# Optimization experiments

Measured on AMD Instinct MI355X. Metric: run time of the kernel, lower is better.

## Reference

```python
import jax, jax.numpy as jnp
import numpy as np

B, T, D = 4, 2048, 2048
HS, NH, NG = 128, 16, 4  # head_size, n_head, n_query_groups
R = NH // NG             # queries per group


def setup_inputs() -> dict:
    key = jax.random.key(0)
    ks = jax.random.split(key, 8)
    s = 0.02
    return {
        "x": jax.random.normal(ks[0], (B, T, D), dtype=jnp.float32),
        "WQ": jax.random.normal(ks[1], (HS * NH, D), dtype=jnp.float32) * s,
        "bQ": jax.random.normal(ks[2], (HS * NH,), dtype=jnp.float32) * s,
        "WK": jax.random.normal(ks[3], (HS * NG, D), dtype=jnp.float32) * s,
        "bK": jax.random.normal(ks[4], (HS * NG,), dtype=jnp.float32) * s,
        "WV": jax.random.normal(ks[5], (HS * NG, D), dtype=jnp.float32) * s,
        "bV": jax.random.normal(ks[6], (HS * NG,), dtype=jnp.float32) * s,
        "proj": jax.random.normal(ks[7], (HS * NH, D), dtype=jnp.float32) * s,
    }


def reference(x, WQ, bQ, WK, bK, WV, bV, proj):
    b, t, _ = x.shape
    # projections (torch Linear: x @ W.T + b)
    Q = x @ WQ.T + bQ                                   # (B,T,NH*HS)
    K = (x @ WK.T + bK).reshape(b, t, NG, HS)           # (B,T,NG,HS)
    V = (x @ WV.T + bV).reshape(b, t, NG, HS)
    # torch .repeat tiles the group axis: [g0..g3, g0..g3, ...]
    K = jnp.tile(K, (1, 1, R, 1)).reshape(b, t, NH * HS)
    V = jnp.tile(V, (1, 1, R, 1)).reshape(b, t, NH * HS)
    # single big-dim attention over the concatenated head dim (as in source)
    scores = jnp.einsum('btd,bsd->bts', Q, K)           # (B,T,T)
    causal = jnp.triu(jnp.ones((t, t), dtype=bool), 1)
    scores = jnp.where(causal[None], -jnp.inf, scores)
    # quirk: divide by sqrt(head_size) AFTER softmax
    attn = jax.nn.softmax(scores, axis=-1) / jnp.sqrt(jnp.float32(HS))
    Z = jnp.einsum('bts,bsd->btd', attn, V)             # (B,T,NH*HS)
    return Z @ proj                                     # (B,T,D)
```

## Files before the change

kernel.cpp:

```cpp
#include <hip/hip_runtime.h>
#include <math.h>

typedef _Float16 h16;
typedef _Float16 f16x8 __attribute__((ext_vector_type(8)));
typedef _Float16 f16x4 __attribute__((ext_vector_type(4)));
typedef float f32x4 __attribute__((ext_vector_type(4)));

enum { EPI_F32 = 0, EPI_SPLIT2 = 1, EPI_VT = 2, EPI_H16 = 3 };

struct GP {
  const h16* Ah; const h16* Al;
  const h16* Bh; const h16* Bl;
  const float* bias;
  float* outF;
  h16* oQh; h16* oQl; h16* oKh; h16* oKl;
  h16* outH;
  int K, lda, ldb, ldc;
  size_t sA, sB, sO;
};

__device__ __forceinline__ f32x4 mfma16(f16x8 a, f16x8 b, f32x4 c) {
  return __builtin_amdgcn_mfma_f32_16x16x32_f16(a, b, c, 0, 0, 0);
}

__device__ __forceinline__ void glds16(const h16* g, h16* l) {
  __builtin_amdgcn_global_load_lds((const __attribute__((address_space(1))) void*)g,
                                   (__attribute__((address_space(3))) void*)l,
                                   16, 0, 0);
}

template<int BM, int BN, int BSPL, int TERMS, int EPI, bool CSKIP, bool KLIM>
__global__ __launch_bounds__(256, 2) void gemm_bt(GP p)
{
  constexpr int BK = 64;
  constexpr bool ASPL = (TERMS >= 2);
  constexpr int WM = BM / 2, WN = BN / 2;
  constexpr int FM = WM / 16, FN = WN / 16;

  const int gx = gridDim.x, gy = gridDim.y;
  int lin = blockIdx.x + gx * blockIdx.y;
  const int nwg = gx * gy;
  if ((nwg & 7) == 0) lin = (lin & 7) * (nwg >> 3) + (lin >> 3);
  const int m0 = (lin / gx) * BM;
  const int n0 = (lin % gx) * BN;
  if (CSKIP && n0 >= m0 + BM) return;
  const int z = blockIdx.z;
  const h16* Ah = p.Ah + (size_t)z * p.sA;
  const h16* Al = ASPL ? p.Al + (size_t)z * p.sA : (const h16*)nullptr;
  const h16* Bh = p.Bh + (size_t)z * p.sB;
  const h16* Bl = BSPL ? p.Bl + (size_t)z * p.sB : (const h16*)nullptr;

  __shared__ h16 sAh[BM * BK];
  __shared__ h16 sAl[ASPL ? BM * BK : 8];
  __shared__ h16 sBh[BN * BK];
  __shared__ h16 sBl[BSPL ? BN * BK : 8];

  const int tid = threadIdx.x;
  const int lane = tid & 63;
  const int w = tid >> 6;
  const int wm = (w >> 1) * WM;
  const int wn = (w & 1) * WN;
  const int fr = lane & 15;
  const int fq = lane >> 4;
  const int lrow = lane >> 3;
  const int lcol = (((lane & 7) ^ lrow) * 8);

  f32x4 acc[FM][FN];
#pragma unroll
  for (int i = 0; i < FM; i++)
#pragma unroll
    for (int j = 0; j < FN; j++) acc[i][j] = f32x4{0.f, 0.f, 0.f, 0.f};

  const int kend = KLIM ? ((m0 + BM < p.K) ? (m0 + BM) : p.K) : p.K;

  for (int k0 = 0; k0 < kend; k0 += BK) {
    __syncthreads();
#pragma unroll
    for (int i = w; i < BM / 8; i += 4)
      glds16(Ah + (size_t)(m0 + i * 8 + lrow) * p.lda + (k0 + lcol), &sAh[i * 512]);
    if constexpr (ASPL) {
#pragma unroll
      for (int i = w; i < BM / 8; i += 4)
        glds16(Al + (size_t)(m0 + i * 8 + lrow) * p.lda + (k0 + lcol), &sAl[i * 512]);
    }
#pragma unroll
    for (int i = w; i < BN / 8; i += 4)
      glds16(Bh + (size_t)(n0 + i * 8 + lrow) * p.ldb + (k0 + lcol), &sBh[i * 512]);
    if constexpr (BSPL) {
#pragma unroll
      for (int i = w; i < BN / 8; i += 4)
        glds16(Bl + (size_t)(n0 + i * 8 + lrow) * p.ldb + (k0 + lcol), &sBl[i * 512]);
    }
    __syncthreads();

#pragma unroll
    for (int ks = 0; ks < 2; ks++) {
      const int swo = (((ks * 4 + fq) ^ (fr & 7)) * 8);
      f16x8 fa[FM], fb[FN];
      f16x8 fal[ASPL ? FM : 1], fbl[BSPL ? FN : 1];
#pragma unroll
      for (int m = 0; m < FM; m++) {
        fa[m] = *(const f16x8*)&sAh[(wm + m * 16 + fr) * BK + swo];
        if constexpr (ASPL)
          fal[m] = *(const f16x8*)&sAl[(wm + m * 16 + fr) * BK + swo];
      }
#pragma unroll
      for (int n = 0; n < FN; n++) {
        fb[n] = *(const f16x8*)&sBh[(wn + n * 16 + fr) * BK + swo];
        if constexpr (BSPL)
          fbl[n] = *(const f16x8*)&sBl[(wn + n * 16 + fr) * BK + swo];
      }
#pragma unroll
      for (int m = 0; m < FM; m++)
#pragma unroll
        for (int n = 0; n < FN; n++) {
          acc[m][n] = mfma16(fa[m], fb[n], acc[m][n]);
          if constexpr (TERMS >= 2) acc[m][n] = mfma16(fal[m], fb[n], acc[m][n]);
          if constexpr (TERMS >= 3) acc[m][n] = mfma16(fa[m], fbl[n], acc[m][n]);
        }
    }
  }

#pragma unroll
  for (int m = 0; m < FM; m++) {
    const int grb = m0 + wm + m * 16 + fq * 4;
#pragma unroll
    for (int n = 0; n < FN; n++) {
      const int gc = n0 + wn + n * 16 + fr;
      if constexpr (EPI == EPI_F32) {
        float* o = p.outF + (size_t)z * p.sO;
#pragma unroll
        for (int r = 0; r < 4; r++)
          o[(size_t)(grb + r) * p.ldc + gc] = acc[m][n][r];
      } else if constexpr (EPI == EPI_SPLIT2) {
        const float bv = p.bias[gc];
#pragma unroll
        for (int r = 0; r < 4; r++) {
          const float v = acc[m][n][r] + bv;
          const h16 h = (h16)v;
          const h16 l = (h16)(v - (float)h);
          const size_t idx = (size_t)(grb + r) * 512;
          if (gc < 512) { p.oQh[idx + gc] = h; p.oQl[idx + gc] = l; }
          else          { p.oKh[idx + gc - 512] = h; p.oKl[idx + gc - 512] = l; }
        }
      } else if constexpr (EPI == EPI_VT) {
        const float bv = p.bias[gc];
        f16x4 pk;
#pragma unroll
        for (int r = 0; r < 4; r++) pk[r] = (h16)(acc[m][n][r] + bv);
        const int bb = grb >> 11;
        const int t  = grb & 2047;
        *(f16x4*)(p.outH + ((size_t)bb * 512 + gc) * 2048 + t) = pk;
      } else {
        h16* o = p.outH + (size_t)z * p.sO;
#pragma unroll
        for (int r = 0; r < 4; r++)
          o[(size_t)(grb + r) * p.ldc + gc] = (h16)acc[m][n][r];
      }
    }
  }
}

__global__ __launch_bounds__(256) void split_x(const float* __restrict__ x,
                                               h16* __restrict__ xh, h16* __restrict__ xl)
{
  const size_t i = ((size_t)blockIdx.x * 256 + threadIdx.x) * 8;
  const float4 a = *(const float4*)(x + i);
  const float4 b = *(const float4*)(x + i + 4);
  const float vv[8] = {a.x, a.y, a.z, a.w, b.x, b.y, b.z, b.w};
  f16x8 h, l;
#pragma unroll
  for (int j = 0; j < 8; j++) {
    const h16 hh = (h16)vv[j];
    h[j] = hh;
    l[j] = (h16)(vv[j] - (float)hh);
  }
  *(f16x8*)(xh + i) = h;
  *(f16x8*)(xl + i) = l;
}

__global__ __launch_bounds__(256) void softmax_row(const float* __restrict__ sc,
                                                   h16* __restrict__ attn)
{
  const int bt = blockIdx.x;
  const int t = bt & 2047;
  const int tid = threadIdx.x;
  const int lane = tid & 63;
  const int wid = tid >> 6;
  const int len = t + 1;
  const size_t rowoff = (size_t)bt * 2048;
  const float* row = sc + rowoff;
  float v[8];
#pragma unroll
  for (int j = 0; j < 8; j++) {
    const int c = tid + (j << 8);
    v[j] = (c < len) ? row[c] : -INFINITY;
  }
  float m = v[0];
#pragma unroll
  for (int j = 1; j < 8; j++) m = fmaxf(m, v[j]);
#pragma unroll
  for (int off = 32; off > 0; off >>= 1) m = fmaxf(m, __shfl_xor(m, off));
  __shared__ float redm[4];
  if (lane == 0) redm[wid] = m;
  __syncthreads();
  m = fmaxf(fmaxf(redm[0], redm[1]), fmaxf(redm[2], redm[3]));
  float e[8];
  float s = 0.f;
#pragma unroll
  for (int j = 0; j < 8; j++) { e[j] = expf(v[j] - m); s += e[j]; }
#pragma unroll
  for (int off = 32; off > 0; off >>= 1) s += __shfl_xor(s, off);
  __shared__ float reds[4];
  if (lane == 0) reds[wid] = s;
  __syncthreads();
  s = reds[0] + reds[1] + reds[2] + reds[3];
  const float inv = 1.f / (s * 11.313708498984761f);
#pragma unroll
  for (int j = 0; j < 8; j++) {
    const int c = tid + (j << 8);
    attn[rowoff + c] = (h16)(e[j] * inv);
  }
}

__global__ __launch_bounds__(256) void prep_wqk(const float* __restrict__ WQ, const float* __restrict__ bQ,
                                                const float* __restrict__ WK, const float* __restrict__ bK,
                                                h16* __restrict__ Wh, h16* __restrict__ Wl,
                                                float* __restrict__ bias)
{
  const int idx = blockIdx.x * 256 + threadIdx.x;
  if (idx >= 1024 * 2048) return;
  const int n = idx >> 11;
  const int k = idx & 2047;
  float v;
  if (n < 512) {
    const int g = n >> 7, e = n & 127;
    const size_t base = (size_t)(128 * g + e) * 2048 + k;
    v = WQ[base] + WQ[base + (size_t)512 * 2048] + WQ[base + (size_t)1024 * 2048]
      + WQ[base + (size_t)1536 * 2048];
  } else {
    v = WK[(size_t)(n - 512) * 2048 + k];
  }
  const h16 h = (h16)v;
  Wh[idx] = h;
  Wl[idx] = (h16)(v - (float)h);
  if (k == 0) {
    if (n < 512) {
      const int g = n >> 7, e = n & 127;
      const int r = 128 * g + e;
      bias[n] = bQ[r] + bQ[r + 512] + bQ[r + 1024] + bQ[r + 1536];
    } else {
      bias[n] = bK[n - 512];
    }
  }
}

__global__ __launch_bounds__(256) void prep_wv(const float* __restrict__ WV, const float* __restrict__ bV,
                                               h16* __restrict__ Wv, float* __restrict__ bias)
{
  const int idx = blockIdx.x * 256 + threadIdx.x;
  if (idx >= 512 * 2048) return;
  Wv[idx] = (h16)WV[idx];
  if ((idx & 2047) == 0) bias[idx >> 11] = bV[idx >> 11];
}

__global__ __launch_bounds__(256) void prep_projT(const float* __restrict__ proj,
                                                  h16* __restrict__ projT)
{
  const int idx = blockIdx.x * 256 + threadIdx.x;
  if (idx >= 2048 * 512 / 4) return;
  const int n = idx >> 9;
  const int o = (idx & 511) << 2;
  const int g = n >> 7, e = n & 127;
  const size_t base = (size_t)(128 * g + e) * 2048 + o;
  const float4 a = *(const float4*)(proj + base);
  const float4 b = *(const float4*)(proj + base + (size_t)512 * 2048);
  const float4 c = *(const float4*)(proj + base + (size_t)1024 * 2048);
  const float4 d = *(const float4*)(proj + base + (size_t)1536 * 2048);
  projT[(size_t)(o + 0) * 512 + n] = (h16)(a.x + b.x + c.x + d.x);
  projT[(size_t)(o + 1) * 512 + n] = (h16)(a.y + b.y + c.y + d.y);
  projT[(size_t)(o + 2) * 512 + n] = (h16)(a.z + b.z + c.z + d.z);
  projT[(size_t)(o + 3) * 512 + n] = (h16)(a.w + b.w + c.w + d.w);
}

extern "C" void kernel_launch(void* const* d_in, const int* in_sizes, int n_in,
                              void* d_out, int out_size, void* d_ws, size_t ws_size,
                              hipStream_t stream)
{
  (void)in_sizes; (void)n_in;
  const float* x    = (const float*)d_in[0];
  const float* WQ   = (const float*)d_in[1];
  const float* bQv  = (const float*)d_in[2];
  const float* WK   = (const float*)d_in[3];
  const float* bKv  = (const float*)d_in[4];
  const float* WV   = (const float*)d_in[5];
  const float* bVv  = (const float*)d_in[6];
  const float* proj = (const float*)d_in[7];
  float* out = (float*)d_out;

  char* ws = (char*)d_ws;
  size_t off = 0;
  auto alloc = [&](size_t bytes) -> void* {
    off = (off + 255) & ~(size_t)255;
    void* p = ws + off;
    off += bytes;
    return p;
  };
  char* xregion = (char*)alloc((size_t)2 * 16777216 * 2);
  h16* xh = (h16*)xregion;
  h16* xl = (h16*)(xregion + (size_t)16777216 * 2);
  float* scores = (float*)xregion;
  h16* attn = (h16*)alloc((size_t)4 * 2048 * 2048 * 2);

  h16* Wqk_h = (h16*)alloc((size_t)1024 * 2048 * 2);
  h16* Wqk_l = (h16*)alloc((size_t)1024 * 2048 * 2);
  h16* Wv    = (h16*)alloc((size_t)512 * 2048 * 2);
  h16* projT = (h16*)alloc((size_t)2048 * 512 * 2);
  float* bias_qk = (float*)alloc(1024 * 4);
  float* bias_v  = (float*)alloc(512 * 4);
  h16* Qh = (h16*)alloc((size_t)8192 * 512 * 2);
  h16* Ql = (h16*)alloc((size_t)8192 * 512 * 2);
  h16* Kh = (h16*)alloc((size_t)8192 * 512 * 2);
  h16* Kl = (h16*)alloc((size_t)8192 * 512 * 2);
  h16* Vt = (h16*)alloc((size_t)4 * 512 * 2048 * 2);
  h16* Zg = (h16*)alloc((size_t)8192 * 512 * 2);
  if (off > ws_size) {
    hipMemsetAsync(d_out, 0x7F, (size_t)out_size * 4, stream);
    return;
  }

  prep_wqk<<<8192, 256, 0, stream>>>(WQ, bQv, WK, bKv, Wqk_h, Wqk_l, bias_qk);
  prep_wv<<<4096, 256, 0, stream>>>(WV, bVv, Wv, bias_v);
  prep_projT<<<1024, 256, 0, stream>>>(proj, projT);
  split_x<<<8192, 256, 0, stream>>>(x, xh, xl);

  {
    GP p{};
    p.Ah = xh; p.Al = xl; p.Bh = Wqk_h; p.Bl = Wqk_l; p.bias = bias_qk;
    p.oQh = Qh; p.oQl = Ql; p.oKh = Kh; p.oKl = Kl;
    p.K = 2048; p.lda = 2048; p.ldb = 2048; p.ldc = 0;
    gemm_bt<128, 128, 1, 3, EPI_SPLIT2, false, false><<<dim3(8, 64, 1), 256, 0, stream>>>(p);
  }
  {
    GP p{};
    p.Ah = xh; p.Bh = Wv; p.bias = bias_v; p.outH = Vt;
    p.K = 2048; p.lda = 2048; p.ldb = 2048; p.ldc = 0;
    gemm_bt<128, 64, 0, 1, EPI_VT, false, false><<<dim3(8, 64, 1), 256, 0, stream>>>(p);
  }
  {
    GP p{};
    p.Ah = Qh; p.Al = Ql; p.Bh = Kh; p.Bl = Kl; p.outF = scores;
    p.K = 512; p.lda = 512; p.ldb = 512; p.ldc = 2048;
    p.sA = (size_t)2048 * 512; p.sB = (size_t)2048 * 512; p.sO = (size_t)2048 * 2048;
    gemm_bt<128, 128, 1, 3, EPI_F32, true, false><<<dim3(16, 16, 4), 256, 0, stream>>>(p);
  }
  softmax_row<<<8192, 256, 0, stream>>>(scores, attn);
  {
    GP p{};
    p.Ah = attn; p.Bh = Vt; p.outH = Zg;
    p.K = 2048; p.lda = 2048; p.ldb = 2048; p.ldc = 512;
    p.sA = (size_t)2048 * 2048; p.sB = (size_t)512 * 2048; p.sO = (size_t)2048 * 512;
    gemm_bt<128, 64, 0, 1, EPI_H16, false, true><<<dim3(8, 16, 4), 256, 0, stream>>>(p);
  }
  {
    GP p{};
    p.Ah = Zg; p.Bh = projT; p.outF = out;
    p.K = 512; p.lda = 512; p.ldb = 512; p.ldc = 2048;
    gemm_bt<128, 128, 0, 1, EPI_F32, false, false><<<dim3(16, 64, 1), 256, 0, stream>>>(p);
  }
}
```

Baseline: 281.8 us.

## Double-buffer LDS tiles in GEMM to overlap global loads with MFMA

Doubles the shared-memory A/B (and split lo) tiles and prefetches the next K tile into the alternate buffer right after the barrier, while MFMAs run on the current buffer. This removes one barrier per iteration and hides global-to-LDS latency behind compute. In exchange, LDS use per block doubles, which may cut the number of resident blocks for the split-precision variants.

```diff
diff --git a/kernel.cpp b/kernel.cpp
--- a/kernel.cpp
+++ b/kernel.cpp
@@ -36,6 +36,7 @@
   constexpr bool ASPL = (TERMS >= 2);
   constexpr int WM = BM / 2, WN = BN / 2;
   constexpr int FM = WM / 16, FN = WN / 16;
+  constexpr int AH = BM * BK, BH = BN * BK;
 
   const int gx = gridDim.x, gy = gridDim.y;
   int lin = blockIdx.x + gx * blockIdx.y;
@@ -50,10 +51,10 @@
   const h16* Bh = p.Bh + (size_t)z * p.sB;
   const h16* Bl = BSPL ? p.Bl + (size_t)z * p.sB : (const h16*)nullptr;
 
-  __shared__ h16 sAh[BM * BK];
-  __shared__ h16 sAl[ASPL ? BM * BK : 8];
-  __shared__ h16 sBh[BN * BK];
-  __shared__ h16 sBl[BSPL ? BN * BK : 8];
+  __shared__ h16 sAh[2 * AH];
+  __shared__ h16 sAl[ASPL ? 2 * AH : 8];
+  __shared__ h16 sBh[2 * BH];
+  __shared__ h16 sBl[BSPL ? 2 * BH : 8];
 
   const int tid = threadIdx.x;
   const int lane = tid & 63;
@@ -72,26 +73,33 @@
     for (int j = 0; j < FN; j++) acc[i][j] = f32x4{0.f, 0.f, 0.f, 0.f};
 
   const int kend = KLIM ? ((m0 + BM < p.K) ? (m0 + BM) : p.K) : p.K;
-
-  for (int k0 = 0; k0 < kend; k0 += BK) {
+  const int nIter = kend / BK;
+
+  auto stage = [&](int k0, int half) {
+    const int ao = half * AH, bo = half * BH;
+#pragma unroll
+    for (int i = w; i < BM / 8; i += 4)
+      glds16(Ah + (size_t)(m0 + i * 8 + lrow) * p.lda + (k0 + lcol), &sAh[ao + i * 512]);
+    if constexpr (ASPL) {
+#pragma unroll
+      for (int i = w; i < BM / 8; i += 4)
+        glds16(Al + (size_t)(m0 + i * 8 + lrow) * p.lda + (k0 + lcol), &sAl[ao + i * 512]);
+    }
+#pragma unroll
+    for (int i = w; i < BN / 8; i += 4)
+      glds16(Bh + (size_t)(n0 + i * 8 + lrow) * p.ldb + (k0 + lcol), &sBh[bo + i * 512]);
+    if constexpr (BSPL) {
+#pragma unroll
+      for (int i = w; i < BN / 8; i += 4)
+        glds16(Bl + (size_t)(n0 + i * 8 + lrow) * p.ldb + (k0 + lcol), &sBl[bo + i * 512]);
+    }
+  };
+
+  stage(0, 0);
+  for (int it = 0; it < nIter; ++it) {
     __syncthreads();
-#pragma unroll
-    for (int i = w; i < BM / 8; i += 4)
-      glds16(Ah + (size_t)(m0 + i * 8 + lrow) * p.lda + (k0 + lcol), &sAh[i * 512]);
-    if constexpr (ASPL) {
-#pragma unroll
-      for (int i = w; i < BM / 8; i += 4)
-        glds16(Al + (size_t)(m0 + i * 8 + lrow) * p.lda + (k0 + lcol), &sAl[i * 512]);
-    }
-#pragma unroll
-    for (int i = w; i < BN / 8; i += 4)
-      glds16(Bh + (size_t)(n0 + i * 8 + lrow) * p.ldb + (k0 + lcol), &sBh[i * 512]);
-    if constexpr (BSPL) {
-#pragma unroll
-      for (int i = w; i < BN / 8; i += 4)
-        glds16(Bl + (size_t)(n0 + i * 8 + lrow) * p.ldb + (k0 + lcol), &sBl[i * 512]);
-    }
-    __syncthreads();
+    if (it + 1 < nIter) stage((it + 1) * BK, (it + 1) & 1);
+    const int ca = (it & 1) * AH, cb = (it & 1) * BH;
 
 #pragma unroll
     for (int ks = 0; ks < 2; ks++) {
@@ -100,15 +108,15 @@
       f16x8 fal[ASPL ? FM : 1], fbl[BSPL ? FN : 1];
 #pragma unroll
       for (int m = 0; m < FM; m++) {
-        fa[m] = *(const f16x8*)&sAh[(wm + m * 16 + fr) * BK + swo];
+        fa[m] = *(const f16x8*)&sAh[ca + (wm + m * 16 + fr) * BK + swo];
         if constexpr (ASPL)
-          fal[m] = *(const f16x8*)&sAl[(wm + m * 16 + fr) * BK + swo];
+          fal[m] = *(const f16x8*)&sAl[ca + (wm + m * 16 + fr) * BK + swo];
       }
 #pragma unroll
       for (int n = 0; n < FN; n++) {
-        fb[n] = *(const f16x8*)&sBh[(wn + n * 16 + fr) * BK + swo];
+        fb[n] = *(const f16x8*)&sBh[cb + (wn + n * 16 + fr) * BK + swo];
         if constexpr (BSPL)
-          fbl[n] = *(const f16x8*)&sBl[(wn + n * 16 + fr) * BK + swo];
+          fbl[n] = *(const f16x8*)&sBl[cb + (wn + n * 16 + fr) * BK + swo];
       }
 #pragma unroll
       for (int m = 0; m < FM; m++)
```

Result: slower. 354.4 us (+25.8%).
